# Performance work log

Hardware: AMD Instinct MI355X
Metric: run time of the kernel (lower is better)

## Reference

```python
import jax, jax.numpy as jnp
import numpy as np


def setup_inputs() -> dict:
    key = jax.random.key(0)
    k1, k2 = jax.random.split(key)
    B, N, M, D = 8, 2048, 2048, 1024
    x = jax.random.normal(k1, (B, N, D), dtype=jnp.float32)
    y = jax.random.normal(k2, (B, M, D), dtype=jnp.float32)
    return {"x": x, "y": y}


def reference(x, y):
    # scores: [B, N, M] = x @ y^T
    scores = jnp.einsum("bnd,bmd->bnm", x, y)
    # row-normalized attention over M (axis=2 of scores)
    attn_row = jax.nn.softmax(scores, axis=2)
    # column-normalized attention: softmax over N of scores^T, i.e. axis=1 then transpose
    attn_col = jax.nn.softmax(scores, axis=1)  # [B, N, M], normalized over N
    A = jnp.einsum("bnm,bmd->bnd", attn_row, y)          # attended summary of y per x-token
    Bout = jnp.einsum("bnm,bnd->bmd", attn_col, x)       # attended summary of x per y-token
    return (A, Bout)
```

## Files before the change

### kernel.cpp

```cpp
#include <hip/hip_runtime.h>
#include <cstdint>
#include <cstddef>

namespace {

constexpr int Bb = 8;
constexpr int Nn = 2048;
constexpr int Dd = 1024;
constexpr int NT = 64;

typedef _Float16 half8 __attribute__((ext_vector_type(8)));
typedef float f32x4v __attribute__((ext_vector_type(4)));
typedef float f32x16v __attribute__((ext_vector_type(16)));
typedef unsigned int v2u __attribute__((ext_vector_type(2)));
typedef unsigned int v4u __attribute__((ext_vector_type(4)));

__device__ __forceinline__ float fast_exp2(float x) {
  float r;
  asm("v_exp_f32 %0, %1\n\ts_nop 1" : "=v"(r) : "v"(x));
  return r;
}

__device__ __forceinline__ unsigned cvt2(float a, float b) {
  return __builtin_bit_cast(unsigned, __builtin_amdgcn_cvt_pkrtz(a, b));
}

__device__ __forceinline__ float quad_max(float v) {
  int a = __builtin_amdgcn_update_dpp(0, __builtin_bit_cast(int, v), 0xB1,
                                      0xF, 0xF, true);
  float m = fmaxf(v, __builtin_bit_cast(float, a));
  int b = __builtin_amdgcn_update_dpp(0, __builtin_bit_cast(int, m), 0x4E,
                                      0xF, 0xF, true);
  return fmaxf(m, __builtin_bit_cast(float, b));
}
__device__ __forceinline__ float quad_add(float v) {
  int a = __builtin_amdgcn_update_dpp(0, __builtin_bit_cast(int, v), 0xB1,
                                      0xF, 0xF, true);
  float s = v + __builtin_bit_cast(float, a);
  int b = __builtin_amdgcn_update_dpp(0, __builtin_bit_cast(int, s), 0x4E,
                                      0xF, 0xF, true);
  return s + __builtin_bit_cast(float, b);
}

__device__ __forceinline__ void barrier_lgkm() {
  asm volatile("s_waitcnt lgkmcnt(0)" ::: "memory");
  __builtin_amdgcn_s_barrier();
  __builtin_amdgcn_sched_barrier(0);
}
__device__ __forceinline__ void barrier_plain() {
  __builtin_amdgcn_s_barrier();
  __builtin_amdgcn_sched_barrier(0);
}

__global__ void convf16(const float* __restrict__ in, v4u* __restrict__ out) {
  const int n8 = Bb * Nn * Dd / 8;
  int i = blockIdx.x * blockDim.x + threadIdx.x;
  const int stride = gridDim.x * blockDim.x;
  const f32x4v* in4 = (const f32x4v*)in;
  for (; i < n8; i += stride) {
    f32x4v a = in4[2 * i], b = in4[2 * i + 1];
    v4u p;
    p[0] = cvt2(a[0], a[1]);
    p[1] = cvt2(a[2], a[3]);
    p[2] = cvt2(b[0], b[1]);
    p[3] = cvt2(b[2], b[3]);
    out[i] = p;
  }
}

template <int WS>
__device__ __forceinline__ v4u ld8h(const float* f32p, const v4u* h16p) {
  if constexpr (WS) {
    return *h16p;
  } else {
    f32x4v a = *(const f32x4v*)f32p;
    f32x4v b = *(const f32x4v*)(f32p + 4);
    v4u p;
    p[0] = cvt2(a[0], a[1]);
    p[1] = cvt2(a[2], a[3]);
    p[2] = cvt2(b[0], b[1]);
    p[3] = cvt2(b[2], b[3]);
    return p;
  }
}

template <int WS>
__global__ __launch_bounds__(512, 2) void flash_fwd(
    const float* __restrict__ Qf, const float* __restrict__ Yf,
    const v4u* __restrict__ Qw, const v4u* __restrict__ Yw,
    float* __restrict__ Om) {
  __shared__ __attribute__((aligned(128))) char ybuf[65536];
  __shared__ __attribute__((aligned(16))) float pscr2[4][32][36];
  __shared__ __attribute__((aligned(16))) char Pb[2048];
  __shared__ float sscale[32];
  __shared__ float sinvl[32];
  __shared__ int sflag[2];

  const int tid = (int)threadIdx.x;
  const int w = tid >> 6, l = tid & 63;
  const int lm = l & 15, g = (l >> 4) & 3, g2 = (l >> 5) & 1, l31 = l & 31;
  const int kvf = w >> 2, ds = w & 3;
  const int bid = (int)blockIdx.x, batch = bid & 7, row0 = (bid >> 3) * 32;
  const size_t bY = (size_t)batch * Nn;

  v4u qreg[2][8];
#pragma unroll
  for (int qh = 0; qh < 2; ++qh)
#pragma unroll
    for (int ks = 0; ks < 8; ++ks) {
      const int rr = row0 + qh * 16 + lm;
      const int dd_ = ds * 256 + ks * 32 + g * 8;
      qreg[qh][ks] = ld8h<WS>(Qf + (size_t)(bY + rr) * Dd + dd_,
                              Qw + (size_t)(bY + rr) * 128 + (dd_ >> 3));
    }

#define LOADY(dst, t_)                                                        \
  do {                                                                        \
    const int rr_ = (t_)*32 + kvf * 16 + lm;                                  \
    _Pragma("unroll") for (int ks = 0; ks < 8; ++ks) {                        \
      const int dd_ = ds * 256 + ks * 32 + g * 8;                             \
      dst[ks] = ld8h<WS>(Yf + (size_t)(bY + rr_) * Dd + dd_,                  \
                         Yw + (size_t)(bY + rr_) * 128 + (dd_ >> 3));         \
    }                                                                         \
  } while (0)

  const unsigned sbase =
      (unsigned)((kvf * 4 + (lm >> 2)) * 8192 + (ds * 16 + (g >> 1)) * 128 +
                 (lm & 3) * 32 + (g & 1) * 16);
#define STAGE_WR(SRC)                                                         \
  do {                                                                        \
    _Pragma("unroll") for (int ks = 0; ks < 8; ++ks)                          \
        *(v4u*)(ybuf + sbase + ks * 256) = SRC[ks];                           \
  } while (0)

  v4u s[8];
  LOADY(s, 0);
  STAGE_WR(s);

  f32x16v Oacc[4];
#pragma unroll
  for (int i = 0; i < 4; ++i)
#pragma unroll
    for (int j = 0; j < 16; ++j) Oacc[i][j] = 0.0f;

  float m_run = -__builtin_inff();
  float l_run = 0.0f;
  const unsigned ylds = (unsigned)(uintptr_t)&ybuf[0];
  constexpr float L2E = 1.44269504088896f;

  v2u trr[16];

#define ISSUE_TR()                                                            \
  do {                                                                        \
    _Pragma("unroll") for (int kb = 0; kb < 2; ++kb)                          \
        _Pragma("unroll") for (int df = 0; df < 4; ++df) {                    \
      const unsigned wb =                                                     \
          ylds + (unsigned)((kb * 4 + g2 * 2) * 8192 +                        \
                            ((w * 4 + df) * 2 + (l31 >> 4)) * 128 +           \
                            (l31 & 15) * 8);                                  \
      asm volatile("ds_read_b64_tr_b16 %0, %1"                                \
                   : "=v"(trr[kb * 8 + df * 2])                               \
                   : "v"(wb));                                                \
      asm volatile("ds_read_b64_tr_b16 %0, %1"                                \
                   : "=v"(trr[kb * 8 + df * 2 + 1])                           \
                   : "v"(wb + 8192u));                                        \
    }                                                                         \
  } while (0)

  __syncthreads();

#define TILE_BODY(t_)                                                         \
  do {                                                                        \
    f32x4v acc0 = {0.f, 0.f, 0.f, 0.f}, acc1 = {0.f, 0.f, 0.f, 0.f};          \
    _Pragma("unroll") for (int ks = 0; ks < 8; ++ks) {                        \
      half8 av = __builtin_bit_cast(half8, s[ks]);                            \
      acc0 = __builtin_amdgcn_mfma_f32_16x16x32_f16(                          \
          av, __builtin_bit_cast(half8, qreg[0][ks]), acc0, 0, 0, 0);         \
      acc1 = __builtin_amdgcn_mfma_f32_16x16x32_f16(                          \
          av, __builtin_bit_cast(half8, qreg[1][ks]), acc1, 0, 0, 0);         \
    }                                                                         \
    LOADY(s, ((t_) + 1) & 63);                                                \
    *(f32x4v*)&pscr2[ds][lm][kvf * 16 + g * 4] = acc0;                        \
    *(f32x4v*)&pscr2[ds][16 + lm][kvf * 16 + g * 4] = acc1;                   \
    barrier_lgkm();                       \
    if (w >= 2) {                                                             \
      ISSUE_TR();                                                             \
    } else {                                                                  \
      __builtin_amdgcn_s_setprio(1);                                          \
      const int rq = w * 16 + (l >> 2);                     \
      const int c = l & 3;                                      \
      f32x4v lo = {0.f, 0.f, 0.f, 0.f}, hi = {0.f, 0.f, 0.f, 0.f};            \
      _Pragma("unroll") for (int s_ = 0; s_ < 4; ++s_) {                      \
        lo += *(const f32x4v*)&pscr2[s_][rq][c * 8];                          \
        hi += *(const f32x4v*)&pscr2[s_][rq][c * 8 + 4];                      \
      }                                                                       \
      float pm = fmaxf(fmaxf(fmaxf(lo[0], lo[1]), fmaxf(lo[2], lo[3])),       \
                       fmaxf(fmaxf(hi[0], hi[1]), fmaxf(hi[2], hi[3])));      \
      pm = quad_max(pm);                                                      \
      bool defer = (pm <= m_run + 8.0f);                                      \
      bool allw = (bool)__all((int)defer);                                    \
      float scale = 1.0f;                                                     \
      if (!allw) {                                                            \
        float mn = fmaxf(m_run, pm);                                          \
        scale = fast_exp2((m_run - mn) * L2E);                                \
        m_run = mn;                                                           \
      }                                                                       \
      f32x4v ea, eb;                                                          \
      _Pragma("unroll") for (int i = 0; i < 4; ++i) {                         \
        ea[i] = fast_exp2((lo[i] - m_run) * L2E);                             \
        eb[i] = fast_exp2((hi[i] - m_run) * L2E);                             \
      }                                                                       \
      float ps = (ea[0] + ea[1]) + (ea[2] + ea[3]) + (eb[0] + eb[1]) +        \
                 (eb[2] + eb[3]);                                             \
      ps = quad_add(ps);                                                      \
      l_run = l_run * scale + ps;                                             \
      v4u pk;                                                                 \
      pk[0] = cvt2(ea[0], ea[1]);                                             \
      pk[1] = cvt2(ea[2], ea[3]);                                             \
      pk[2] = cvt2(eb[0], eb[1]);                                             \
      pk[3] = cvt2(eb[2], eb[3]);                                             \
      *(v4u*)(Pb + c * 512 + rq * 16) = pk;                                   \
      if (c == 0) sscale[rq] = scale;                                         \
      if (l == 0) sflag[w] = allw ? 0 : 1;                                    \
      __builtin_amdgcn_s_setprio(0);                                          \
      ISSUE_TR();                                                             \
    }                                                                         \
    barrier_lgkm();               \
    half8 pa0 = *(const half8*)(Pb + g2 * 512 + l31 * 16);                    \
    half8 pa1 = *(const half8*)(Pb + (2 + g2) * 512 + l31 * 16);              \
    if (sflag[0] | sflag[1]) {                                                \
      _Pragma("unroll") for (int df = 0; df < 4; ++df)                        \
          _Pragma("unroll") for (int r = 0; r < 16; ++r) {                    \
        const int q_ = (r & 3) + 8 * (r >> 2) + 4 * g2;                       \
        Oacc[df][r] *= sscale[q_];                                            \
      }                                                                       \
    }                                                                         \
    asm volatile("s_waitcnt lgkmcnt(0)" ::: "memory");                        \
    __builtin_amdgcn_sched_barrier(0);                                        \
    _Pragma("unroll") for (int kb = 0; kb < 2; ++kb)                          \
        _Pragma("unroll") for (int df = 0; df < 4; ++df) {                    \
      v4u bu;                                                                 \
      bu[0] = trr[kb * 8 + df * 2][0];                                        \
      bu[1] = trr[kb * 8 + df * 2][1];                                        \
      bu[2] = trr[kb * 8 + df * 2 + 1][0];                                    \
      bu[3] = trr[kb * 8 + df * 2 + 1][1];                                    \
      Oacc[df] = __builtin_amdgcn_mfma_f32_32x32x16_f16(                      \
          kb ? pa1 : pa0, __builtin_bit_cast(half8, bu), Oacc[df], 0, 0, 0);  \
    }                                                                         \
    barrier_plain();                \
    STAGE_WR(s);                                                              \
  } while (0)

  for (int t = 0; t < NT; ++t) {
    TILE_BODY(t);
  }

  if (w < 2 && (l & 3) == 0) sinvl[w * 16 + (l >> 2)] = 1.0f / l_run;
  __syncthreads();
#pragma unroll
  for (int df = 0; df < 4; ++df)
#pragma unroll
    for (int r = 0; r < 16; ++r) {
      const int q_ = (r & 3) + 8 * (r >> 2) + 4 * g2;
      const float inv = sinvl[q_];
      Om[(size_t)(bY + row0 + q_) * Dd + (w * 4 + df) * 32 + l31] =
          Oacc[df][r] * inv;
    }
#undef TILE_BODY
#undef ISSUE_TR
#undef STAGE_WR
#undef LOADY
}

}

extern "C" void kernel_launch(void* const* d_in, const int* in_sizes, int n_in,
                              void* d_out, int out_size, void* d_ws,
                              size_t ws_size, hipStream_t stream) {
  (void)in_sizes; (void)n_in; (void)out_size;
  const float* x = (const float*)d_in[0];
  const float* y = (const float*)d_in[1];
  float* A = (float*)d_out;
  float* Bo = A + (size_t)Bb * Nn * Dd;
  const size_t halfws = (size_t)Bb * Nn * Dd * 2;
  dim3 fg(512), fb(512);
  if (d_ws != nullptr && ws_size >= 2 * halfws) {
    v4u* Xw = (v4u*)d_ws;
    v4u* Yw = (v4u*)((char*)d_ws + halfws);
    hipLaunchKernelGGL(convf16, dim3(2048), dim3(256), 0, stream, x, Xw);
    hipLaunchKernelGGL(convf16, dim3(2048), dim3(256), 0, stream, y, Yw);
    hipLaunchKernelGGL(flash_fwd<1>, fg, fb, 0, stream, x, y, Xw, Yw, A);
    hipLaunchKernelGGL(flash_fwd<1>, fg, fb, 0, stream, y, x, Yw, Xw, Bo);
  } else {
    hipLaunchKernelGGL(flash_fwd<0>, fg, fb, 0, stream, x, y, (const v4u*)x,
                       (const v4u*)y, A);
    hipLaunchKernelGGL(flash_fwd<0>, fg, fb, 0, stream, y, x, (const v4u*)y,
                       (const v4u*)x, Bo);
  }
}
```

Before: 542.4 us.

## Split attention blocks to 16 query rows with four waves and 16x16 PV MFMA

Reworks the fused attention kernel so each block processes 16 query rows with 256 threads instead of 32 rows with 512, doubling the grid. Each wave now loads both 16-row halves of the Y tile and the PV product uses 16x16x32 MFMAs with two batches of transposed LDS reads. The intent is more blocks and less per-block synchronisation across eight waves. The trade-off is halved reuse of each staged Y tile, doubling total Y traffic, and a single softmax wave that serialises more work.

Result: slower. 985.0 us (+81.6%).

```diff
diff --git a/kernel.cpp b/kernel.cpp
--- a/kernel.cpp
+++ b/kernel.cpp
@@ -11,7 +11,6 @@
 
 typedef _Float16 half8 __attribute__((ext_vector_type(8)));
 typedef float f32x4v __attribute__((ext_vector_type(4)));
-typedef float f32x16v __attribute__((ext_vector_type(16)));
 typedef unsigned int v2u __attribute__((ext_vector_type(2)));
 typedef unsigned int v4u __attribute__((ext_vector_type(4)));
 
@@ -85,188 +84,195 @@
 }
 
 template <int WS>
-__global__ __launch_bounds__(512, 2) void flash_fwd(
+__global__ __launch_bounds__(256, 2) void flash_fwd(
     const float* __restrict__ Qf, const float* __restrict__ Yf,
     const v4u* __restrict__ Qw, const v4u* __restrict__ Yw,
     float* __restrict__ Om) {
   __shared__ __attribute__((aligned(128))) char ybuf[65536];
-  __shared__ __attribute__((aligned(16))) float pscr2[4][32][36];
-  __shared__ __attribute__((aligned(16))) char Pb[2048];
-  __shared__ float sscale[32];
-  __shared__ float sinvl[32];
-  __shared__ int sflag[2];
+  __shared__ __attribute__((aligned(16))) float pscr2[4][16][36];
+  __shared__ __attribute__((aligned(16))) char Pb[1024];
+  __shared__ float sscale[16];
+  __shared__ float sinvl[16];
+  __shared__ int sflag[1];
 
   const int tid = (int)threadIdx.x;
   const int w = tid >> 6, l = tid & 63;
-  const int lm = l & 15, g = (l >> 4) & 3, g2 = (l >> 5) & 1, l31 = l & 31;
-  const int kvf = w >> 2, ds = w & 3;
-  const int bid = (int)blockIdx.x, batch = bid & 7, row0 = (bid >> 3) * 32;
+  const int lm = l & 15, g = (l >> 4) & 3;
+  const int bid = (int)blockIdx.x, batch = bid & 7, row0 = (bid >> 3) * 16;
   const size_t bY = (size_t)batch * Nn;
 
-  v4u qreg[2][8];
-#pragma unroll
-  for (int qh = 0; qh < 2; ++qh)
-#pragma unroll
-    for (int ks = 0; ks < 8; ++ks) {
-      const int rr = row0 + qh * 16 + lm;
-      const int dd_ = ds * 256 + ks * 32 + g * 8;
-      qreg[qh][ks] = ld8h<WS>(Qf + (size_t)(bY + rr) * Dd + dd_,
-                              Qw + (size_t)(bY + rr) * 128 + (dd_ >> 3));
-    }
-
-#define LOADY(dst, t_)                                                        \
+  v4u qreg[8];
+#pragma unroll
+  for (int ks = 0; ks < 8; ++ks) {
+    const int rr = row0 + lm;
+    const int dd_ = w * 256 + ks * 32 + g * 8;
+    qreg[ks] = ld8h<WS>(Qf + (size_t)(bY + rr) * Dd + dd_,
+                        Qw + (size_t)(bY + rr) * 128 + (dd_ >> 3));
+  }
+
+  v4u s[2][8];
+#define LOADY(t_)                                                             \
   do {                                                                        \
-    const int rr_ = (t_)*32 + kvf * 16 + lm;                                  \
-    _Pragma("unroll") for (int ks = 0; ks < 8; ++ks) {                        \
-      const int dd_ = ds * 256 + ks * 32 + g * 8;                             \
-      dst[ks] = ld8h<WS>(Yf + (size_t)(bY + rr_) * Dd + dd_,                  \
-                         Yw + (size_t)(bY + rr_) * 128 + (dd_ >> 3));         \
+    _Pragma("unroll") for (int h = 0; h < 2; ++h)                             \
+        _Pragma("unroll") for (int ks = 0; ks < 8; ++ks) {                    \
+      const int rr_ = (t_)*32 + h * 16 + lm;                                  \
+      const int dd_ = w * 256 + ks * 32 + g * 8;                              \
+      s[h][ks] = ld8h<WS>(Yf + (size_t)(bY + rr_) * Dd + dd_,                 \
+                          Yw + (size_t)(bY + rr_) * 128 + (dd_ >> 3));        \
     }                                                                         \
   } while (0)
 
   const unsigned sbase =
-      (unsigned)((kvf * 4 + (lm >> 2)) * 8192 + (ds * 16 + (g >> 1)) * 128 +
+      (unsigned)((lm >> 2) * 8192 + (w * 16 + (g >> 1)) * 128 +
                  (lm & 3) * 32 + (g & 1) * 16);
-#define STAGE_WR(SRC)                                                         \
+#define STAGE_WR()                                                            \
   do {                                                                        \
-    _Pragma("unroll") for (int ks = 0; ks < 8; ++ks)                          \
-        *(v4u*)(ybuf + sbase + ks * 256) = SRC[ks];                           \
+    _Pragma("unroll") for (int h = 0; h < 2; ++h)                             \
+        _Pragma("unroll") for (int ks = 0; ks < 8; ++ks)                      \
+        *(v4u*)(ybuf + sbase + h * 32768u + ks * 256) = s[h][ks];             \
   } while (0)
 
-  v4u s[8];
-  LOADY(s, 0);
-  STAGE_WR(s);
-
-  f32x16v Oacc[4];
-#pragma unroll
-  for (int i = 0; i < 4; ++i)
-#pragma unroll
-    for (int j = 0; j < 16; ++j) Oacc[i][j] = 0.0f;
+  LOADY(0);
+  STAGE_WR();
+
+  f32x4v Oacc[16];
+#pragma unroll
+  for (int i = 0; i < 16; ++i)
+#pragma unroll
+    for (int j = 0; j < 4; ++j) Oacc[i][j] = 0.0f;
 
   float m_run = -__builtin_inff();
   float l_run = 0.0f;
   const unsigned ylds = (unsigned)(uintptr_t)&ybuf[0];
   constexpr float L2E = 1.44269504088896f;
 
-  v2u trr[16];
-
-#define ISSUE_TR()                                                            \
+#define ISSUE_TR(dst, SB)                                                     \
   do {                                                                        \
-    _Pragma("unroll") for (int kb = 0; kb < 2; ++kb)                          \
-        _Pragma("unroll") for (int df = 0; df < 4; ++df) {                    \
-      const unsigned wb =                                                     \
-          ylds + (unsigned)((kb * 4 + g2 * 2) * 8192 +                        \
-                            ((w * 4 + df) * 2 + (l31 >> 4)) * 128 +           \
-                            (l31 & 15) * 8);                                  \
+    _Pragma("unroll") for (int sub = 0; sub < 8; ++sub) {                     \
+      const unsigned a0 = ylds + (unsigned)((2 * g) * 8192 +                  \
+                                            (w * 16 + (SB) + sub) * 128 +    \
+                                            lm * 8);                          \
       asm volatile("ds_read_b64_tr_b16 %0, %1"                                \
-                   : "=v"(trr[kb * 8 + df * 2])                               \
-                   : "v"(wb));                                                \
+                   : "=v"(dst[sub * 2])                                       \
+                   : "v"(a0));                                                \
       asm volatile("ds_read_b64_tr_b16 %0, %1"                                \
-                   : "=v"(trr[kb * 8 + df * 2 + 1])                           \
-                   : "v"(wb + 8192u));                                        \
+                   : "=v"(dst[sub * 2 + 1])                                   \
+                   : "v"(a0 + 8192u));                                        \
     }                                                                         \
   } while (0)
 
   __syncthreads();
 
-#define TILE_BODY(t_)                                                         \
-  do {                                                                        \
-    f32x4v acc0 = {0.f, 0.f, 0.f, 0.f}, acc1 = {0.f, 0.f, 0.f, 0.f};          \
-    _Pragma("unroll") for (int ks = 0; ks < 8; ++ks) {                        \
-      half8 av = __builtin_bit_cast(half8, s[ks]);                            \
-      acc0 = __builtin_amdgcn_mfma_f32_16x16x32_f16(                          \
-          av, __builtin_bit_cast(half8, qreg[0][ks]), acc0, 0, 0, 0);         \
-      acc1 = __builtin_amdgcn_mfma_f32_16x16x32_f16(                          \
-          av, __builtin_bit_cast(half8, qreg[1][ks]), acc1, 0, 0, 0);         \
-    }                                                                         \
-    LOADY(s, ((t_) + 1) & 63);                                                \
-    *(f32x4v*)&pscr2[ds][lm][kvf * 16 + g * 4] = acc0;                        \
-    *(f32x4v*)&pscr2[ds][16 + lm][kvf * 16 + g * 4] = acc1;                   \
-    barrier_lgkm();                       \
-    if (w >= 2) {                                                             \
-      ISSUE_TR();                                                             \
-    } else {                                                                  \
-      __builtin_amdgcn_s_setprio(1);                                          \
-      const int rq = w * 16 + (l >> 2);                     \
-      const int c = l & 3;                                      \
-      f32x4v lo = {0.f, 0.f, 0.f, 0.f}, hi = {0.f, 0.f, 0.f, 0.f};            \
-      _Pragma("unroll") for (int s_ = 0; s_ < 4; ++s_) {                      \
-        lo += *(const f32x4v*)&pscr2[s_][rq][c * 8];                          \
-        hi += *(const f32x4v*)&pscr2[s_][rq][c * 8 + 4];                      \
-      }                                                                       \
-      float pm = fmaxf(fmaxf(fmaxf(lo[0], lo[1]), fmaxf(lo[2], lo[3])),       \
-                       fmaxf(fmaxf(hi[0], hi[1]), fmaxf(hi[2], hi[3])));      \
-      pm = quad_max(pm);                                                      \
-      bool defer = (pm <= m_run + 8.0f);                                      \
-      bool allw = (bool)__all((int)defer);                                    \
-      float scale = 1.0f;                                                     \
-      if (!allw) {                                                            \
-        float mn = fmaxf(m_run, pm);                                          \
-        scale = fast_exp2((m_run - mn) * L2E);                                \
-        m_run = mn;                                                           \
-      }                                                                       \
-      f32x4v ea, eb;                                                          \
-      _Pragma("unroll") for (int i = 0; i < 4; ++i) {                         \
-        ea[i] = fast_exp2((lo[i] - m_run) * L2E);                             \
-        eb[i] = fast_exp2((hi[i] - m_run) * L2E);                             \
-      }                                                                       \
-      float ps = (ea[0] + ea[1]) + (ea[2] + ea[3]) + (eb[0] + eb[1]) +        \
-                 (eb[2] + eb[3]);                                             \
-      ps = quad_add(ps);                                                      \
-      l_run = l_run * scale + ps;                                             \
-      v4u pk;                                                                 \
-      pk[0] = cvt2(ea[0], ea[1]);                                             \
-      pk[1] = cvt2(ea[2], ea[3]);                                             \
-      pk[2] = cvt2(eb[0], eb[1]);                                             \
-      pk[3] = cvt2(eb[2], eb[3]);                                             \
-      *(v4u*)(Pb + c * 512 + rq * 16) = pk;                                   \
-      if (c == 0) sscale[rq] = scale;                                         \
-      if (l == 0) sflag[w] = allw ? 0 : 1;                                    \
-      __builtin_amdgcn_s_setprio(0);                                          \
-      ISSUE_TR();                                                             \
-    }                                                                         \
-    barrier_lgkm();               \
-    half8 pa0 = *(const half8*)(Pb + g2 * 512 + l31 * 16);                    \
-    half8 pa1 = *(const half8*)(Pb + (2 + g2) * 512 + l31 * 16);              \
-    if (sflag[0] | sflag[1]) {                                                \
-      _Pragma("unroll") for (int df = 0; df < 4; ++df)                        \
-          _Pragma("unroll") for (int r = 0; r < 16; ++r) {                    \
-        const int q_ = (r & 3) + 8 * (r >> 2) + 4 * g2;                       \
-        Oacc[df][r] *= sscale[q_];                                            \
-      }                                                                       \
-    }                                                                         \
-    asm volatile("s_waitcnt lgkmcnt(0)" ::: "memory");                        \
-    __builtin_amdgcn_sched_barrier(0);                                        \
-    _Pragma("unroll") for (int kb = 0; kb < 2; ++kb)                          \
-        _Pragma("unroll") for (int df = 0; df < 4; ++df) {                    \
-      v4u bu;                                                                 \
-      bu[0] = trr[kb * 8 + df * 2][0];                                        \
-      bu[1] = trr[kb * 8 + df * 2][1];                                        \
-      bu[2] = trr[kb * 8 + df * 2 + 1][0];                                    \
-      bu[3] = trr[kb * 8 + df * 2 + 1][1];                                    \
-      Oacc[df] = __builtin_amdgcn_mfma_f32_32x32x16_f16(                      \
-          kb ? pa1 : pa0, __builtin_bit_cast(half8, bu), Oacc[df], 0, 0, 0);  \
-    }                                                                         \
-    barrier_plain();                \
-    STAGE_WR(s);                                                              \
-  } while (0)
-
   for (int t = 0; t < NT; ++t) {
-    TILE_BODY(t);
-  }
-
-  if (w < 2 && (l & 3) == 0) sinvl[w * 16 + (l >> 2)] = 1.0f / l_run;
+    f32x4v acc0 = {0.f, 0.f, 0.f, 0.f}, acc1 = {0.f, 0.f, 0.f, 0.f};
+#pragma unroll
+    for (int ks = 0; ks < 8; ++ks) {
+      acc0 = __builtin_amdgcn_mfma_f32_16x16x32_f16(
+          __builtin_bit_cast(half8, s[0][ks]), __builtin_bit_cast(half8, qreg[ks]),
+          acc0, 0, 0, 0);
+      acc1 = __builtin_amdgcn_mfma_f32_16x16x32_f16(
+          __builtin_bit_cast(half8, s[1][ks]), __builtin_bit_cast(half8, qreg[ks]),
+          acc1, 0, 0, 0);
+    }
+    LOADY((t + 1) & 63);
+    *(f32x4v*)&pscr2[w][lm][g * 4] = acc0;
+    *(f32x4v*)&pscr2[w][lm][16 + g * 4] = acc1;
+    barrier_lgkm();
+
+    v2u trrA[16];
+    if (w == 0) {
+      __builtin_amdgcn_s_setprio(1);
+      const int rq = l >> 2;
+      const int c = l & 3;
+      f32x4v lo = {0.f, 0.f, 0.f, 0.f}, hi = {0.f, 0.f, 0.f, 0.f};
+#pragma unroll
+      for (int s_ = 0; s_ < 4; ++s_) {
+        lo += *(const f32x4v*)&pscr2[s_][rq][c * 8];
+        hi += *(const f32x4v*)&pscr2[s_][rq][c * 8 + 4];
+      }
+      float pm = fmaxf(fmaxf(fmaxf(lo[0], lo[1]), fmaxf(lo[2], lo[3])),
+                       fmaxf(fmaxf(hi[0], hi[1]), fmaxf(hi[2], hi[3])));
+      pm = quad_max(pm);
+      bool defer = (pm <= m_run + 8.0f);
+      bool allw = (bool)__all((int)defer);
+      float scale = 1.0f;
+      if (!allw) {
+        float mn = fmaxf(m_run, pm);
+        scale = fast_exp2((m_run - mn) * L2E);
+        m_run = mn;
+      }
+      f32x4v ea, eb;
+#pragma unroll
+      for (int i = 0; i < 4; ++i) {
+        ea[i] = fast_exp2((lo[i] - m_run) * L2E);
+        eb[i] = fast_exp2((hi[i] - m_run) * L2E);
+      }
+      float ps = (ea[0] + ea[1]) + (ea[2] + ea[3]) + (eb[0] + eb[1]) +
+                 (eb[2] + eb[3]);
+      ps = quad_add(ps);
+      l_run = l_run * scale + ps;
+      v4u pk;
+      pk[0] = cvt2(ea[0], ea[1]);
+      pk[1] = cvt2(ea[2], ea[3]);
+      pk[2] = cvt2(eb[0], eb[1]);
+      pk[3] = cvt2(eb[2], eb[3]);
+      *(v4u*)(Pb + c * 256 + rq * 16) = pk;
+      if (c == 0) sscale[rq] = scale;
+      if (l == 0) sflag[0] = allw ? 0 : 1;
+      __builtin_amdgcn_s_setprio(0);
+      ISSUE_TR(trrA, 0);
+    } else {
+      ISSUE_TR(trrA, 0);
+    }
+    barrier_lgkm();
+
+    half8 pa = *(const half8*)(Pb + g * 256 + lm * 16);
+    if (sflag[0]) {
+#pragma unroll
+      for (int sub = 0; sub < 16; ++sub)
+#pragma unroll
+        for (int r = 0; r < 4; ++r) Oacc[sub][r] *= sscale[g * 4 + r];
+    }
+    asm volatile("s_waitcnt lgkmcnt(0)" ::: "memory");
+    __builtin_amdgcn_sched_barrier(0);
+#pragma unroll
+    for (int sub = 0; sub < 8; ++sub) {
+      v4u bu;
+      bu[0] = trrA[sub * 2][0];
+      bu[1] = trrA[sub * 2][1];
+      bu[2] = trrA[sub * 2 + 1][0];
+      bu[3] = trrA[sub * 2 + 1][1];
+      Oacc[sub] = __builtin_amdgcn_mfma_f32_16x16x32_f16(
+          pa, __builtin_bit_cast(half8, bu), Oacc[sub], 0, 0, 0);
+    }
+    v2u trrB[16];
+    ISSUE_TR(trrB, 8);
+    asm volatile("s_waitcnt lgkmcnt(0)" ::: "memory");
+    __builtin_amdgcn_sched_barrier(0);
+#pragma unroll
+    for (int sub = 0; sub < 8; ++sub) {
+      v4u bu;
+      bu[0] = trrB[sub * 2][0];
+      bu[1] = trrB[sub * 2][1];
+      bu[2] = trrB[sub * 2 + 1][0];
+      bu[3] = trrB[sub * 2 + 1][1];
+      Oacc[8 + sub] = __builtin_amdgcn_mfma_f32_16x16x32_f16(
+          pa, __builtin_bit_cast(half8, bu), Oacc[8 + sub], 0, 0, 0);
+    }
+    barrier_plain();
+    STAGE_WR();
+  }
+
+  if (w == 0 && (l & 3) == 0) sinvl[l >> 2] = 1.0f / l_run;
   __syncthreads();
 #pragma unroll
-  for (int df = 0; df < 4; ++df)
-#pragma unroll
-    for (int r = 0; r < 16; ++r) {
-      const int q_ = (r & 3) + 8 * (r >> 2) + 4 * g2;
-      const float inv = sinvl[q_];
-      Om[(size_t)(bY + row0 + q_) * Dd + (w * 4 + df) * 32 + l31] =
-          Oacc[df][r] * inv;
-    }
-#undef TILE_BODY
+  for (int sub = 0; sub < 16; ++sub)
+#pragma unroll
+    for (int r = 0; r < 4; ++r) {
+      const int q_ = g * 4 + r;
+      Om[(size_t)(bY + row0 + q_) * Dd + w * 256 + sub * 16 + lm] =
+          Oacc[sub][r] * sinvl[q_];
+    }
 #undef ISSUE_TR
 #undef STAGE_WR
 #undef LOADY
@@ -283,7 +289,7 @@
   float* A = (float*)d_out;
   float* Bo = A + (size_t)Bb * Nn * Dd;
   const size_t halfws = (size_t)Bb * Nn * Dd * 2;
-  dim3 fg(512), fb(512);
+  dim3 fg(Bb * (Nn / 16)), fb(256);
   if (d_ws != nullptr && ws_size >= 2 * halfws) {
     v4u* Xw = (v4u*)d_ws;
     v4u* Yw = (v4u*)((char*)d_ws + halfws);
```

## Spread per-tile softmax across all eight waves instead of two

Applied to the files above, without the earlier changes.

The online-softmax step for each KV tile (partial-sum reduction, max, exp, row sum, P packing) previously ran on only two waves, with the other six idle apart from issuing transposed loads. It now runs on all eight waves: each wave handles four rows, with 16 lanes per row, and reductions use a 16-lane DPP tree. The per-wave rescale flags grow to eight entries, read back as two vector loads. This shortens the serial softmax critical path between barriers, but adds extra DPP steps and removes the priority boost, and the transpose loads now issue after the softmax in every wave.

Result: no change. 547.6 us (+1.0%).

```diff
diff --git a/kernel.cpp b/kernel.cpp
--- a/kernel.cpp
+++ b/kernel.cpp
@@ -10,6 +10,7 @@
 constexpr int NT = 64;
 
 typedef _Float16 half8 __attribute__((ext_vector_type(8)));
+typedef float f32x2v __attribute__((ext_vector_type(2)));
 typedef float f32x4v __attribute__((ext_vector_type(4)));
 typedef float f32x16v __attribute__((ext_vector_type(16)));
 typedef unsigned int v2u __attribute__((ext_vector_type(2)));
@@ -25,21 +26,25 @@
   return __builtin_bit_cast(unsigned, __builtin_amdgcn_cvt_pkrtz(a, b));
 }
 
-__device__ __forceinline__ float quad_max(float v) {
-  int a = __builtin_amdgcn_update_dpp(0, __builtin_bit_cast(int, v), 0xB1,
-                                      0xF, 0xF, true);
-  float m = fmaxf(v, __builtin_bit_cast(float, a));
-  int b = __builtin_amdgcn_update_dpp(0, __builtin_bit_cast(int, m), 0x4E,
-                                      0xF, 0xF, true);
-  return fmaxf(m, __builtin_bit_cast(float, b));
-}
-__device__ __forceinline__ float quad_add(float v) {
-  int a = __builtin_amdgcn_update_dpp(0, __builtin_bit_cast(int, v), 0xB1,
-                                      0xF, 0xF, true);
-  float s = v + __builtin_bit_cast(float, a);
-  int b = __builtin_amdgcn_update_dpp(0, __builtin_bit_cast(int, s), 0x4E,
-                                      0xF, 0xF, true);
-  return s + __builtin_bit_cast(float, b);
+template <int CTRL>
+__device__ __forceinline__ float dpp_f(float v) {
+  return __builtin_bit_cast(
+      float, __builtin_amdgcn_update_dpp(0, __builtin_bit_cast(int, v), CTRL,
+                                         0xF, 0xF, true));
+}
+__device__ __forceinline__ float red16_max(float v) {
+  v = fmaxf(v, dpp_f<0xB1>(v));
+  v = fmaxf(v, dpp_f<0x4E>(v));
+  v = fmaxf(v, dpp_f<0x124>(v));
+  v = fmaxf(v, dpp_f<0x128>(v));
+  return v;
+}
+__device__ __forceinline__ float red16_add(float v) {
+  v = v + dpp_f<0xB1>(v);
+  v = v + dpp_f<0x4E>(v);
+  v = v + dpp_f<0x124>(v);
+  v = v + dpp_f<0x128>(v);
+  return v;
 }
 
 __device__ __forceinline__ void barrier_lgkm() {
@@ -94,7 +99,7 @@
   __shared__ __attribute__((aligned(16))) char Pb[2048];
   __shared__ float sscale[32];
   __shared__ float sinvl[32];
-  __shared__ int sflag[2];
+  __shared__ __attribute__((aligned(16))) int sflag8[8];
 
   const int tid = (int)threadIdx.x;
   const int w = tid >> 6, l = tid & 63;
@@ -183,20 +188,16 @@
     *(f32x4v*)&pscr2[ds][lm][kvf * 16 + g * 4] = acc0;                        \
     *(f32x4v*)&pscr2[ds][16 + lm][kvf * 16 + g * 4] = acc1;                   \
     barrier_lgkm();                       \
-    if (w >= 2) {                                                             \
-      ISSUE_TR();                                                             \
-    } else {                                                                  \
-      __builtin_amdgcn_s_setprio(1);                                          \
-      const int rq = w * 16 + (l >> 2);                     \
-      const int c = l & 3;                                      \
-      f32x4v lo = {0.f, 0.f, 0.f, 0.f}, hi = {0.f, 0.f, 0.f, 0.f};            \
-      _Pragma("unroll") for (int s_ = 0; s_ < 4; ++s_) {                      \
-        lo += *(const f32x4v*)&pscr2[s_][rq][c * 8];                          \
-        hi += *(const f32x4v*)&pscr2[s_][rq][c * 8 + 4];                      \
+    {                   \
+      const int rq = 4 * w + (l >> 4);                             \
+      const int c = l & 15;                      \
+      float s0 = 0.f, s1 = 0.f;                                               \
+      _Pragma("unroll") for (int sl = 0; sl < 4; ++sl) {                      \
+        f32x2v p_ = *(const f32x2v*)&pscr2[sl][rq][2 * c];                    \
+        s0 += p_[0];                                                          \
+        s1 += p_[1];                                                          \
       }                                                                       \
-      float pm = fmaxf(fmaxf(fmaxf(lo[0], lo[1]), fmaxf(lo[2], lo[3])),       \
-                       fmaxf(fmaxf(hi[0], hi[1]), fmaxf(hi[2], hi[3])));      \
-      pm = quad_max(pm);                                                      \
+      float pm = red16_max(fmaxf(s0, s1));                                    \
       bool defer = (pm <= m_run + 8.0f);                                      \
       bool allw = (bool)__all((int)defer);                                    \
       float scale = 1.0f;                                                     \
@@ -205,30 +206,22 @@
         scale = fast_exp2((m_run - mn) * L2E);                                \
         m_run = mn;                                                           \
       }                                                                       \
-      f32x4v ea, eb;                                                          \
-      _Pragma("unroll") for (int i = 0; i < 4; ++i) {                         \
-        ea[i] = fast_exp2((lo[i] - m_run) * L2E);                             \
-        eb[i] = fast_exp2((hi[i] - m_run) * L2E);                             \
-      }                                                                       \
-      float ps = (ea[0] + ea[1]) + (ea[2] + ea[3]) + (eb[0] + eb[1]) +        \
-                 (eb[2] + eb[3]);                                             \
-      ps = quad_add(ps);                                                      \
+      float e0 = fast_exp2((s0 - m_run) * L2E);                               \
+      float e1 = fast_exp2((s1 - m_run) * L2E);                               \
+      float ps = red16_add(e0 + e1);                                          \
       l_run = l_run * scale + ps;                                             \
-      v4u pk;                                                                 \
-      pk[0] = cvt2(ea[0], ea[1]);                                             \
-      pk[1] = cvt2(ea[2], ea[3]);                                             \
-      pk[2] = cvt2(eb[0], eb[1]);                                             \
-      pk[3] = cvt2(eb[2], eb[3]);                                             \
-      *(v4u*)(Pb + c * 512 + rq * 16) = pk;                                   \
+      *(unsigned*)(Pb + (c >> 2) * 512 + rq * 16 + (c & 3) * 4) =             \
+          cvt2(e0, e1);                                                       \
       if (c == 0) sscale[rq] = scale;                                         \
-      if (l == 0) sflag[w] = allw ? 0 : 1;                                    \
-      __builtin_amdgcn_s_setprio(0);                                          \
-      ISSUE_TR();                                                             \
-    }                                                                         \
+      if (l == 0) sflag8[w] = allw ? 0 : 1;                                   \
+    }                                                                         \
+    ISSUE_TR();                                                               \
     barrier_lgkm();               \
     half8 pa0 = *(const half8*)(Pb + g2 * 512 + l31 * 16);                    \
     half8 pa1 = *(const half8*)(Pb + (2 + g2) * 512 + l31 * 16);              \
-    if (sflag[0] | sflag[1]) {                                                \
+    v4u f0 = *(const v4u*)&sflag8[0];                                         \
+    v4u f1 = *(const v4u*)&sflag8[4];                                         \
+    if (f0[0] | f0[1] | f0[2] | f0[3] | f1[0] | f1[1] | f1[2] | f1[3]) {      \
       _Pragma("unroll") for (int df = 0; df < 4; ++df)                        \
           _Pragma("unroll") for (int r = 0; r < 16; ++r) {                    \
         const int q_ = (r & 3) + 8 * (r >> 2) + 4 * g2;                       \
@@ -255,7 +248,7 @@
     TILE_BODY(t);
   }
 
-  if (w < 2 && (l & 3) == 0) sinvl[w * 16 + (l >> 2)] = 1.0f / l_run;
+  if ((l & 15) == 0) sinvl[4 * w + (l >> 4)] = 1.0f / l_run;
   __syncthreads();
 #pragma unroll
   for (int df = 0; df < 4; ++df)
```
